# Kernel tuning notes

Hardware: AMD Instinct MI355X
Metric: run time of the kernel (lower is better)

Reference implementation:

```python
import jax, jax.numpy as jnp
import numpy as np

B, F, V, DW, H, K, T = 32, 2048, 12000, 300, 512, 3, 32
START_ID, END_ID = 1, 2
NEG = -1e9


def lstm(x, h, c, Wx, Wh, b):
    # BasicLSTMCell with forget_bias=1.0
    z = x @ Wx + h @ Wh + b  # [N, 4H]
    i, f, g, o = jnp.split(z, 4, axis=-1)
    c2 = jax.nn.sigmoid(f + 1.0) * c + jax.nn.sigmoid(i) * jnp.tanh(g)
    h2 = jax.nn.sigmoid(o) * jnp.tanh(c2)
    return h2, c2


def beam_decode(E, Wx, Wh, b, Wl, bl, img):
    Bn = img.shape[0]
    img_t = jnp.repeat(img, K, axis=0)  # tile_batch: [B*K, F]
    h = jnp.zeros((Bn * K, H), img.dtype)
    c = jnp.zeros_like(h)
    beam_lp = jnp.tile(jnp.array([0.0] + [NEG] * (K - 1), img.dtype), (Bn, 1))  # [B,K]
    prev = jnp.full((Bn, K), START_ID, jnp.int32)
    finished = jnp.zeros((Bn, K), bool)
    lengths = jnp.zeros((Bn, K), jnp.int32)
    ids = jnp.zeros((Bn, K, T), jnp.int32)
    end_row = jnp.where(jnp.arange(V) == END_ID, 0.0, NEG)  # finished beams only emit END

    def step(carry, t):
        h, c, beam_lp, prev, finished, lengths, ids = carry
        x = jnp.concatenate([E[prev.reshape(-1)], img_t], axis=-1)  # [B*K, DW+F]
        h2, c2 = lstm(x, h, c, Wx, Wh, b)
        lp = jax.nn.log_softmax(h2 @ Wl + bl).reshape(Bn, K, V)
        lp = jnp.where(finished[:, :, None], end_row, lp)
        total = (beam_lp[:, :, None] + lp).reshape(Bn, K * V)
        scores, idx = jax.lax.top_k(total, K)  # [B,K]
        parent = idx // V
        word = (idx % V).astype(jnp.int32)
        g2 = lambda a: jnp.take_along_axis(a, parent, axis=1)
        g3 = lambda a: jnp.take_along_axis(a, parent[:, :, None], axis=1)
        h2 = g3(h2.reshape(Bn, K, H)).reshape(Bn * K, H)
        c2 = g3(c2.reshape(Bn, K, H)).reshape(Bn * K, H)
        ids = g3(ids).at[:, :, t].set(word)  # reorder hypotheses, append word
        fin_p = g2(finished)
        len_p = g2(lengths)
        lengths = jnp.where(fin_p, len_p, len_p + 1)
        finished = fin_p | (word == END_ID)
        return (h2, c2, scores, word, finished, lengths, ids), None

    carry, _ = jax.lax.scan(step, (h, c, beam_lp, prev, finished, lengths, ids), jnp.arange(T))
    return carry[6], carry[5]  # ids [B,K,T], lengths [B,K]


def teacher_rnn(E, Wx, Wh, b, img_t, seq_inputs, lengths):
    # dynamic_rnn semantics: zero outputs and frozen state past sequence_length
    N, L = seq_inputs.shape
    emb = E[seq_inputs]  # [N, L, DW]
    h0 = jnp.zeros((N, H), E.dtype)
    c0 = jnp.zeros_like(h0)

    def step(carry, xs):
        h, c = carry
        x_t, t = xs
        xin = jnp.concatenate([x_t, img_t], axis=-1)
        h2, c2 = lstm(xin, h, c, Wx, Wh, b)
        active = (t < lengths)[:, None]
        h = jnp.where(active, h2, h)
        c = jnp.where(active, c2, c)
        return (h, c), jnp.where(active, h2, 0.0)

    _, outs = jax.lax.scan(step, (h0, c0), (emb.transpose(1, 0, 2), jnp.arange(L)))
    return outs.transpose(1, 0, 2)  # [N, L, H]


def setup_inputs() -> dict:
    key = jax.random.key(0)
    ks = jax.random.split(key, 6)
    return {
        "mean_image_features": jax.random.normal(ks[0], (B, F), jnp.float32),
        "embeddings": jax.random.normal(ks[1], (V, DW), jnp.float32) * 0.1,
        "Wx": jax.random.normal(ks[2], (DW + F, 4 * H), jnp.float32) / np.sqrt(DW + F),
        "Wh": jax.random.normal(ks[3], (H, 4 * H), jnp.float32) / np.sqrt(H),
        "b_lstm": jnp.zeros((4 * H,), jnp.float32),
        "W_logits": jax.random.normal(ks[4], (H, V), jnp.float32) / np.sqrt(H),
        "b_logits": jnp.zeros((V,), jnp.float32),
    }


def reference(mean_image_features, embeddings, Wx, Wh, b_lstm, W_logits, b_logits):
    Bn = mean_image_features.shape[0]
    ids, lengths = beam_decode(embeddings, Wx, Wh, b_lstm, W_logits, b_logits, mean_image_features)
    seq_inputs = jnp.concatenate(
        [jnp.full((Bn, K, 1), START_ID, jnp.int32), ids], axis=2
    ).reshape(Bn * K, T + 1)
    img_t = jnp.repeat(mean_image_features, K, axis=0)
    acts = teacher_rnn(embeddings, Wx, Wh, b_lstm, img_t, seq_inputs, lengths.reshape(-1))
    logits = (acts @ W_logits + b_logits).reshape(Bn, K, T + 1, V)
    return logits, jnp.argmax(logits, axis=-1).astype(jnp.int32)
```

## Files before the change

### kernel.cpp

```cpp
#include <hip/hip_runtime.h>
#include <hip/hip_bf16.h>
#include <math.h>

#define NB   32
#define FDIM 2048
#define VV   12000
#define DWW  300
#define HH   512
#define KW   3
#define TDEC 32
#define SEQ  33
#define NK   96
#define G4   2048
#define START_ID 1
#define END_ID   2
#define NROWS 3168
#define NLB   188
#define INTMX 0x7fffffff
#define FLOORF (-3.0e38f)
#define BAR_STRIDE 512
#define SHARD 64

typedef float f4v __attribute__((ext_vector_type(4)));
__device__ __forceinline__ void nt_store4(float* p, float4 v){
  f4v t; t.x=v.x; t.y=v.y; t.z=v.z; t.w=v.w;
  __builtin_nontemporal_store(t, (f4v*)p);
}

__device__ __forceinline__ float sigf(float x){ return 1.0f/(1.0f+expf(-x)); }

__device__ __forceinline__ unsigned short f2b(float x){
  __hip_bfloat16 b = __float2bfloat16(x);
  return *reinterpret_cast<unsigned short*>(&b);
}

__device__ __forceinline__ void ins3(float v, int i, float tv[3], int ti[3]){
  if (v > tv[0] || (v == tv[0] && i < ti[0])){
    tv[2]=tv[1]; ti[2]=ti[1]; tv[1]=tv[0]; ti[1]=ti[0]; tv[0]=v; ti[0]=i;
  } else if (v > tv[1] || (v == tv[1] && i < ti[1])){
    tv[2]=tv[1]; ti[2]=ti[1]; tv[1]=v; ti[1]=i;
  } else if (v > tv[2] || (v == tv[2] && i < ti[2])){
    tv[2]=v; ti[2]=i;
  }
}

__device__ __forceinline__ void flag_arrive(int* f, int bid){
  __hip_atomic_fetch_add(f + (bid&7)*SHARD, 1, __ATOMIC_RELEASE, __HIP_MEMORY_SCOPE_AGENT);
}
__device__ __forceinline__ void flag_wait(int* f, int target){
  if (threadIdx.x < 64){
    int lane = threadIdx.x;
    for (;;){
      int x = (lane<8) ? __hip_atomic_load(f + lane*SHARD, __ATOMIC_ACQUIRE, __HIP_MEMORY_SCOPE_AGENT) : 0;
      x += __shfl_xor(x,1); x += __shfl_xor(x,2); x += __shfl_xor(x,4);
      if (__shfl(x,0) >= target) break;
      __builtin_amdgcn_s_sleep(4);
    }
  }
  __syncthreads();
}

struct SArgs {
  const float *E, *Wx, *Wh, *Wl, *blog;
  float *P, *c2, *h2s, *zp, *partA, *beam_lp, *rowamax;
  int *prev, *finished, *lengths, *parst;
  int *cnt0, *cnt1;
  void *Lst;
};

__global__ __launch_bounds__(128) void k_pimg(const float* __restrict__ img,
                                              const float* __restrict__ Wx,
                                              float* __restrict__ parts)
{
  int colb = blockIdx.x, fb = blockIdx.y, tid = threadIdx.x;
  int col = colb*128 + tid;
  int f0 = fb*128;
  __shared__ float s_img[32][128];
  for (int r=0;r<32;r++) s_img[r][tid] = img[r*FDIM + f0 + tid];
  __syncthreads();
  float acc[32];
  #pragma unroll
  for (int r=0;r<32;r++) acc[r]=0.f;
  for (int f2=0; f2<128; ++f2){
    float w = Wx[(size_t)(DWW + f0 + f2)*G4 + col];
    #pragma unroll
    for (int r=0;r<32;r++) acc[r] += w * s_img[r][f2];
  }
  #pragma unroll
  for (int r=0;r<32;r++) parts[(size_t)fb*(32*G4) + r*G4 + col] = acc[r];
}

__global__ __launch_bounds__(512) void k_prep(const float* __restrict__ parts,
    const float* __restrict__ bls, const float* __restrict__ blog,
    float* __restrict__ P, float* __restrict__ beam_lp, int* __restrict__ prev,
    int* __restrict__ finished, int* __restrict__ lengths, int* __restrict__ cnts,
    float* __restrict__ bamax)
{
  int bid = blockIdx.x, tid = threadIdx.x;
  int gid = bid*512 + tid;
  float s = bls[gid & (G4-1)];
  for (int fb=0; fb<16; ++fb) s += parts[(size_t)fb*(32*G4) + gid];
  P[gid] = s;
  if (gid < 2*TDEC*BAR_STRIDE) cnts[gid] = 0;
  if (bid==0 && tid<NK){
    beam_lp[tid] = (tid%KW==0)?0.f:-1e9f;
    prev[tid]=START_ID; finished[tid]=0; lengths[tid]=0;
  }
  if (bid==2){
    __shared__ float s_rf[8]; __shared__ int s_ri[8];
    float bv=FLOORF; int bi=INTMX;
    for (int i=tid;i<VV;i+=512){
      float v=blog[i];
      if (v>bv || (v==bv && i<bi)){ bv=v; bi=i; }
    }
    #pragma unroll
    for (int d=1;d<64;d<<=1){
      float ov=__shfl_xor(bv,d); int oi=__shfl_xor(bi,d);
      if (ov>bv || (ov==bv && oi<bi)){ bv=ov; bi=oi; }
    }
    if ((tid&63)==0){ s_rf[tid>>6]=bv; s_ri[tid>>6]=bi; }
    __syncthreads();
    if (tid==0){
      for (int w=1;w<8;w++)
        if (s_rf[w]>bv || (s_rf[w]==bv && s_ri[w]<bi)){ bv=s_rf[w]; bi=s_ri[w]; }
      bamax[0] = (float)bi;
    }
  }
}

__global__ __launch_bounds__(512) void k_step1(SArgs a, int t)
{
  int bid = blockIdx.x, tid = threadIdx.x;
  __shared__ float smem[96*17 + 16*64];
  __shared__ int sprev[NK], spar[NK];
  if (t>0 && tid<NK){ sprev[tid]=a.prev[tid]; spar[tid]=a.parst[(t-1)*NK+tid]; }
  __syncthreads();

  {
    int colblk = bid & 31, p = bid >> 5;
    int col0 = colblk*64;
    int ks = p*104, ke = ks+104; if (ke>812) ke=812;
    float* sA = smem;
    float* sB = smem + 96*17;
    int tx = tid&15, ty = tid>>4;
    float4 acc[3];
    #pragma unroll
    for (int r=0;r<3;r++) acc[r]=make_float4(0.f,0.f,0.f,0.f);
    for (int k0=ks;k0<ke;k0+=16){
      int bk = ke-k0; if (bk>16) bk=16;
      for (int i=tid;i<96*16;i+=512){
        int n=i>>4, kk=i&15;
        float v=0.f;
        if (kk<bk){
          int kg=k0+kk;
          if (kg<DWW){
            int w = (t==0)?START_ID:sprev[n];
            v = a.E[(size_t)w*DWW+kg];
          } else if (t>0){
            v = a.h2s[((size_t)(t-1)*NK + spar[n])*HH + (kg-DWW)];
          }
        }
        sA[n*17+kk]=v;
      }
      for (int i=tid;i<16*64;i+=512){
        int kk=i>>6, cc=i&63;
        float v=0.f;
        if (kk<bk){
          int kg=k0+kk;
          v = (kg<DWW) ? a.Wx[(size_t)kg*G4+col0+cc] : a.Wh[(size_t)(kg-DWW)*G4+col0+cc];
        }
        sB[i]=v;
      }
      __syncthreads();
      #pragma unroll
      for (int kk=0;kk<16;++kk){
        float4 b4 = *(const float4*)&sB[kk*64+tx*4];
        #pragma unroll
        for (int rr=0;rr<3;rr++){
          float av = sA[(ty+rr*32)*17+kk];
          acc[rr].x += av*b4.x; acc[rr].y += av*b4.y;
          acc[rr].z += av*b4.z; acc[rr].w += av*b4.w;
        }
      }
      __syncthreads();
    }
    float* zpp = a.zp + (size_t)p*NK*G4;
    #pragma unroll
    for (int rr=0;rr<3;rr++)
      *(float4*)&zpp[(size_t)(ty+rr*32)*G4 + col0 + tx*4] = acc[rr];
  }
  __syncthreads();
  if (tid==0) flag_arrive(&a.cnt0[t*BAR_STRIDE], bid);
  if (bid >= NK) return;

  flag_wait(&a.cnt0[t*BAR_STRIDE], 256);
  {
    int n = bid, m = tid, bb = n/KW;
    const float* Pr = a.P + (size_t)bb*G4;
    float zi=Pr[m], zf=Pr[HH+m], zg=Pr[2*HH+m], zo=Pr[3*HH+m];
    for (int p=0;p<8;p++){
      const float* zz = a.zp + (size_t)p*NK*G4 + (size_t)n*G4;
      zi+=zz[m]; zf+=zz[HH+m]; zg+=zz[2*HH+m]; zo+=zz[3*HH+m];
    }
    float cold = (t==0) ? 0.f : a.c2[(size_t)((t-1)&1)*NK*HH + (size_t)spar[n]*HH + m];
    float c2v = sigf(zf+1.0f)*cold + sigf(zi)*tanhf(zg);
    float h2v = sigf(zo)*tanhf(c2v);
    a.c2[(size_t)(t&1)*NK*HH + (size_t)n*HH + m] = c2v;
    a.h2s[((size_t)t*NK+n)*HH + m] = h2v;
  }
}

template<int BF>
__global__ __launch_bounds__(512) void k_step2(SArgs a, int t)
{
  int bid = blockIdx.x, tid = threadIdx.x;
  __shared__ float smem[96*36 + 32*64];
  __shared__ float s_lse[KW], s_tv3[KW*3];
  __shared__ int   s_ti3[KW*3];

  {
    int col0 = bid*64;
    float* sA = smem;
    float* sB = smem + 96*36;
    int tx=tid&15, ty=tid>>4;
    float4 acc[3];
    #pragma unroll
    for (int r=0;r<3;r++) acc[r]=make_float4(0.f,0.f,0.f,0.f);
    for (int k0=0;k0<HH;k0+=32){
      for (int i=tid;i<768;i+=512){
        int row=i>>3, kq=(i&7)*4;
        *(float4*)&sA[row*36+kq] = *(const float4*)&a.h2s[((size_t)t*NK+row)*HH + k0+kq];
      }
      {
        int kk=tid>>4, c4=(tid&15)*4;
        int col=col0+c4;
        float4 v = make_float4(0.f,0.f,0.f,0.f);
        if (col < VV) v = *(const float4*)&a.Wl[(size_t)(k0+kk)*VV+col];
        *(float4*)&sB[kk*64+c4]=v;
      }
      __syncthreads();
      #pragma unroll
      for (int kk=0;kk<32;++kk){
        float4 b4 = *(const float4*)&sB[kk*64+tx*4];
        #pragma unroll
        for (int rr=0;rr<3;rr++){
          float av = sA[(ty+rr*32)*36+kk];
          acc[rr].x += av*b4.x; acc[rr].y += av*b4.y;
          acc[rr].z += av*b4.z; acc[rr].w += av*b4.w;
        }
      }
      __syncthreads();
    }
    int colg = col0 + tx*4;
    bool cval = colg < VV;
    float4 bias = make_float4(0.f,0.f,0.f,0.f);
    if (cval) bias = *(const float4*)&a.blog[colg];
    #pragma unroll
    for (int rr=0;rr<3;rr++){
      int row = ty + rr*32;
      float v0,v1,v2,v3;
      if (cval){
        v0=acc[rr].x+bias.x; v1=acc[rr].y+bias.y;
        v2=acc[rr].z+bias.z; v3=acc[rr].w+bias.w;
        size_t off = (size_t)(t*NK+row)*VV + colg;
        if (BF){
          ushort4 u;
          u.x=f2b(v0); u.y=f2b(v1); u.z=f2b(v2); u.w=f2b(v3);
          *(ushort4*)((unsigned short*)a.Lst + off) = u;
        } else {
          *(float4*)((float*)a.Lst + off) = make_float4(v0,v1,v2,v3);
        }
      } else { v0=v1=v2=v3=-INFINITY; }
      float m = fmaxf(fmaxf(v0,v1),fmaxf(v2,v3));
      #pragma unroll
      for (int d=1;d<16;d<<=1) m = fmaxf(m,__shfl_xor(m,d));
      float tv[3]={-INFINITY,-INFINITY,-INFINITY};
      int   ti[3]={INTMX,INTMX,INTMX};
      float s=0.f;
      if (cval){
        ins3(v0,colg,tv,ti); ins3(v1,colg+1,tv,ti);
        ins3(v2,colg+2,tv,ti); ins3(v3,colg+3,tv,ti);
        s = expf(v0-m)+expf(v1-m)+expf(v2-m)+expf(v3-m);
      }
      #pragma unroll
      for (int d=1;d<16;d<<=1){
        s += __shfl_xor(s,d);
        float p0=__shfl_xor(tv[0],d),p1=__shfl_xor(tv[1],d),p2=__shfl_xor(tv[2],d);
        int q0=__shfl_xor(ti[0],d),q1=__shfl_xor(ti[1],d),q2=__shfl_xor(ti[2],d);
        ins3(p0,q0,tv,ti); ins3(p1,q1,tv,ti); ins3(p2,q2,tv,ti);
      }
      if (tx==0){
        float* rp = a.partA + ((size_t)row*NLB + bid)*8;
        *(float4*)rp = make_float4(m,s,tv[0],tv[1]);
        *((float4*)rp+1) = make_float4(tv[2],__int_as_float(ti[0]),__int_as_float(ti[1]),__int_as_float(ti[2]));
      }
    }
  }
  __syncthreads();
  if (tid==0) flag_arrive(&a.cnt1[t*BAR_STRIDE], bid);
  if (bid >= NB) return;

  flag_wait(&a.cnt1[t*BAR_STRIDE], NLB);
  {
    int b = bid;
    int wv = tid>>6, lane = tid&63;
    if (wv < KW){
      int n = b*KW+wv;
      float M=FLOORF, S=0.f;
      float tv[3]={FLOORF,FLOORF,FLOORF}; int ti[3]={INTMX,INTMX,INTMX};
      for (int i=lane;i<NLB;i+=64){
        const float* rp = a.partA + ((size_t)n*NLB+i)*8;
        float4 r0=*(const float4*)rp, r1=*((const float4*)rp+1);
        float nm = fmaxf(M,r0.x);
        S = S*expf(M-nm) + r0.y*expf(r0.x-nm);
        M = nm;
        ins3(r0.z,__float_as_int(r1.y),tv,ti);
        ins3(r0.w,__float_as_int(r1.z),tv,ti);
        ins3(r1.x,__float_as_int(r1.w),tv,ti);
      }
      #pragma unroll
      for (int d=1;d<64;d<<=1){
        float Mo=__shfl_xor(M,d), So=__shfl_xor(S,d);
        float nm=fmaxf(M,Mo);
        S = S*expf(M-nm)+So*expf(Mo-nm);
        M=nm;
        float p0=__shfl_xor(tv[0],d),p1=__shfl_xor(tv[1],d),p2=__shfl_xor(tv[2],d);
        int q0=__shfl_xor(ti[0],d),q1=__shfl_xor(ti[1],d),q2=__shfl_xor(ti[2],d);
        ins3(p0,q0,tv,ti); ins3(p1,q1,tv,ti); ins3(p2,q2,tv,ti);
      }
      if (lane==0){
        s_lse[wv] = M + logf(S);
        #pragma unroll
        for (int j=0;j<3;j++){ s_tv3[wv*3+j]=tv[j]; s_ti3[wv*3+j]=ti[j]; }
        a.rowamax[t*NK+n] = (float)ti[0];
      }
    }
    __syncthreads();
    if (tid==0){
      float cv[3]={FLOORF,FLOORF,FLOORF}; int cf[3]={INTMX,INTMX,INTMX};
      for (int k=0;k<KW;k++){
        int n=b*KW+k;
        if (a.finished[n]){
          ins3(a.beam_lp[n], k*VV+END_ID, cv,cf);
        } else {
          float blp=a.beam_lp[n], lse=s_lse[k];
          for (int j=0;j<3;j++)
            ins3(blp + (s_tv3[k*3+j]-lse), k*VV+s_ti3[k*3+j], cv,cf);
        }
      }
      int fin_old[KW], len_old[KW];
      for (int j=0;j<KW;j++){ fin_old[j]=a.finished[b*KW+j]; len_old[j]=a.lengths[b*KW+j]; }
      for (int kp=0;kp<KW;kp++){
        int par=cf[kp]/VV, word=cf[kp]-par*VV;
        a.beam_lp[b*KW+kp]=cv[kp];
        a.prev[b*KW+kp]=word;
        a.parst[t*NK + b*KW+kp] = b*KW+par;
        int fp=fin_old[par];
        a.lengths[b*KW+kp] = fp?len_old[par]:(len_old[par]+1);
        a.finished[b*KW+kp] = fp | (word==END_ID);
      }
    }
  }
}

__global__ __launch_bounds__(128) void k_backtrack(const int* __restrict__ parst,
                                                   const int* __restrict__ lengths,
                                                   int* __restrict__ rowsrc)
{
  int n = threadIdx.x;
  if (n >= NK) return;
  int b = n / KW;
  int len = lengths[n];
  rowsrc[n*SEQ + TDEC] = -1;
  int a = n;
  for (int tau = TDEC-1; tau >= 1; --tau){
    int p = parst[tau*NK + a];
    rowsrc[n*SEQ + tau] = (tau < len) ? (tau*NK + p) : -1;
    a = p;
  }
  rowsrc[n*SEQ + 0] = b*KW;
}

template<int BF>
__global__ __launch_bounds__(512) void k_gather(const void* __restrict__ Lst,
    const int* __restrict__ rowsrc, const float* __restrict__ rowamax,
    const float* __restrict__ bamax, const float* __restrict__ blog,
    float* __restrict__ out)
{
  int row = blockIdx.x, tid = threadIdx.x;
  int src = rowsrc[row];
  float* orow = out + (size_t)row*VV;
  if (src >= 0){
    if (BF){
      const unsigned short* L = (const unsigned short*)Lst + (size_t)src*VV;
      for (int j=tid;j<VV/4;j+=512){
        ushort4 u = *(const ushort4*)&L[j*4];
        float4 v;
        v.x = __uint_as_float(((unsigned)u.x)<<16);
        v.y = __uint_as_float(((unsigned)u.y)<<16);
        v.z = __uint_as_float(((unsigned)u.z)<<16);
        v.w = __uint_as_float(((unsigned)u.w)<<16);
        nt_store4(&orow[j*4], v);
      }
    } else {
      const float* L = (const float*)Lst + (size_t)src*VV;
      for (int j=tid;j<VV/4;j+=512){
        float4 v = *(const float4*)&L[j*4];
        nt_store4(&orow[j*4], v);
      }
    }
    if (tid==0) out[(size_t)NROWS*VV + row] = rowamax[src];
  } else {
    for (int j=tid;j<VV/4;j+=512){
      float4 v = *(const float4*)&blog[j*4];
      nt_store4(&orow[j*4], v);
    }
    if (tid==0) out[(size_t)NROWS*VV + row] = bamax[0];
  }
}

extern "C" void kernel_launch(void* const* d_in, const int* in_sizes, int n_in,
                              void* d_out, int out_size, void* d_ws, size_t ws_size,
                              hipStream_t stream) {
  (void)in_sizes; (void)n_in; (void)out_size;
  const float* img  = (const float*)d_in[0];
  const float* E    = (const float*)d_in[1];
  const float* Wx   = (const float*)d_in[2];
  const float* Wh   = (const float*)d_in[3];
  const float* bls  = (const float*)d_in[4];
  const float* Wl   = (const float*)d_in[5];
  const float* blog = (const float*)d_in[6];
  float* out = (float*)d_out;

  float* ws = (float*)d_ws;
  size_t o = 0;
  float* P       = ws+o; o += (size_t)NB*G4;
  float* c2      = ws+o; o += (size_t)2*NK*HH;
  float* h2s     = ws+o; o += (size_t)TDEC*NK*HH;
  float* zp      = ws+o; o += (size_t)8*NK*G4;
  float* partA   = ws+o; o += (size_t)NK*NLB*8;
  float* beam_lp = ws+o; o += 128;
  float* rowamax = ws+o; o += (size_t)TDEC*NK;
  float* bamax   = ws+o; o += 4;
  int* prev      = (int*)(ws+o); o += 128;
  int* finished  = (int*)(ws+o); o += 128;
  int* lengths   = (int*)(ws+o); o += 128;
  int* parst     = (int*)(ws+o); o += (size_t)TDEC*NK;
  int* rowsrc    = (int*)(ws+o); o += 3328;
  int* cnts      = (int*)(ws+o); o += (size_t)2*TDEC*BAR_STRIDE;
  o = (o+3) & ~(size_t)3;
  void* Lst      = (void*)(ws+o);

  bool f32 = (ws_size/4 > o) && ((ws_size/4 - o) >= (size_t)TDEC*NK*VV);

  SArgs a;
  a.E=E; a.Wx=Wx; a.Wh=Wh; a.Wl=Wl; a.blog=blog;
  a.P=P; a.c2=c2; a.h2s=h2s; a.zp=zp; a.partA=partA;
  a.beam_lp=beam_lp; a.rowamax=rowamax;
  a.prev=prev; a.finished=finished; a.lengths=lengths; a.parst=parst;
  a.cnt0=cnts; a.cnt1=cnts+TDEC*BAR_STRIDE;
  a.Lst=Lst;

  k_pimg<<<dim3(16,16),128,0,stream>>>(img, Wx, zp);
  k_prep<<<128,512,0,stream>>>(zp, bls, blog, P, beam_lp, prev, finished, lengths, cnts, bamax);

  if (f32){
    for (int t=0;t<TDEC;t++){
      k_step1<<<256,512,0,stream>>>(a,t);
      k_step2<0><<<NLB,512,0,stream>>>(a,t);
    }
    k_backtrack<<<1,128,0,stream>>>(parst, lengths, rowsrc);
    k_gather<0><<<NROWS,512,0,stream>>>(Lst,rowsrc,rowamax,bamax,blog,out);
  } else {
    for (int t=0;t<TDEC;t++){
      k_step1<<<256,512,0,stream>>>(a,t);
      k_step2<1><<<NLB,512,0,stream>>>(a,t);
    }
    k_backtrack<<<1,128,0,stream>>>(parst, lengths, rowsrc);
    k_gather<1><<<NROWS,512,0,stream>>>(Lst,rowsrc,rowamax,bamax,blog,out);
  }
}
```

Measured before the change: 2.961 ms.

## Fuse per-step LSTM and logits kernels into one launch with flag barriers

Merges k_step1 and k_step2 into a single k_step kernel per decode step. The two stages are now joined by an in-kernel atomic flag barrier instead of a kernel boundary, and the backtrack is folded into the last step behind another barrier. This drops 33 kernel launches and their inter-kernel gaps. The flag-wait loop now polls with relaxed loads and a shorter sleep, then does one acquire load at the end. The cost is a larger shared-memory footprint for the fused kernel and reliance on all 188 participating blocks being co-resident to avoid deadlock.

Measured after the change: 3.093 ms. 4.5% more time.

```diff
diff --git a/kernel.cpp b/kernel.cpp
--- a/kernel.cpp
+++ b/kernel.cpp
@@ -20,6 +20,7 @@
 #define FLOORF (-3.0e38f)
 #define BAR_STRIDE 512
 #define SHARD 64
+#define NBAR (3*TDEC+1)
 
 typedef float f4v __attribute__((ext_vector_type(4)));
 __device__ __forceinline__ void nt_store4(float* p, float4 v){
@@ -51,11 +52,12 @@
   if (threadIdx.x < 64){
     int lane = threadIdx.x;
     for (;;){
-      int x = (lane<8) ? __hip_atomic_load(f + lane*SHARD, __ATOMIC_ACQUIRE, __HIP_MEMORY_SCOPE_AGENT) : 0;
+      int x = (lane<8) ? __hip_atomic_load(f + lane*SHARD, __ATOMIC_RELAXED, __HIP_MEMORY_SCOPE_AGENT) : 0;
       x += __shfl_xor(x,1); x += __shfl_xor(x,2); x += __shfl_xor(x,4);
       if (__shfl(x,0) >= target) break;
-      __builtin_amdgcn_s_sleep(4);
-    }
+      __builtin_amdgcn_s_sleep(2);
+    }
+    if (lane==0) (void)__hip_atomic_load(f, __ATOMIC_ACQUIRE, __HIP_MEMORY_SCOPE_AGENT);
   }
   __syncthreads();
 }
@@ -63,8 +65,8 @@
 struct SArgs {
   const float *E, *Wx, *Wh, *Wl, *blog;
   float *P, *c2, *h2s, *zp, *partA, *beam_lp, *rowamax;
-  int *prev, *finished, *lengths, *parst;
-  int *cnt0, *cnt1;
+  int *prev, *finished, *lengths, *parst, *rowsrc;
+  int *cnts;
   void *Lst;
 };
 
@@ -101,7 +103,7 @@
   float s = bls[gid & (G4-1)];
   for (int fb=0; fb<16; ++fb) s += parts[(size_t)fb*(32*G4) + gid];
   P[gid] = s;
-  if (gid < 2*TDEC*BAR_STRIDE) cnts[gid] = 0;
+  if (gid < NBAR*BAR_STRIDE) cnts[gid] = 0;
   if (bid==0 && tid<NK){
     beam_lp[tid] = (tid%KW==0)?0.f:-1e9f;
     prev[tid]=START_ID; finished[tid]=0; lengths[tid]=0;
@@ -128,11 +130,19 @@
   }
 }
 
-__global__ __launch_bounds__(512) void k_step1(SArgs a, int t)
+template<int BF>
+__global__ __launch_bounds__(512) void k_step(SArgs a, int t)
 {
   int bid = blockIdx.x, tid = threadIdx.x;
-  __shared__ float smem[96*17 + 16*64];
+  __shared__ float smem[96*36 + 32*64];
   __shared__ int sprev[NK], spar[NK];
+  __shared__ float s_lse[KW], s_tv3[KW*3];
+  __shared__ int   s_ti3[KW*3];
+  int* bZ = a.cnts + (size_t)(t*3+0)*BAR_STRIDE;
+  int* bG = a.cnts + (size_t)(t*3+1)*BAR_STRIDE;
+  int* bL = a.cnts + (size_t)(t*3+2)*BAR_STRIDE;
+  int* bS = a.cnts + (size_t)(3*TDEC)*BAR_STRIDE;
+
   if (t>0 && tid<NK){ sprev[tid]=a.prev[tid]; spar[tid]=a.parst[(t-1)*NK+tid]; }
   __syncthreads();
 
@@ -190,11 +200,11 @@
       *(float4*)&zpp[(size_t)(ty+rr*32)*G4 + col0 + tx*4] = acc[rr];
   }
   __syncthreads();
-  if (tid==0) flag_arrive(&a.cnt0[t*BAR_STRIDE], bid);
-  if (bid >= NK) return;
-
-  flag_wait(&a.cnt0[t*BAR_STRIDE], 256);
-  {
+  if (tid==0) flag_arrive(bZ, bid);
+  if (bid >= NLB) return;
+
+  if (bid < NK){
+    flag_wait(bZ, 256);
     int n = bid, m = tid, bb = n/KW;
     const float* Pr = a.P + (size_t)bb*G4;
     float zi=Pr[m], zf=Pr[HH+m], zg=Pr[2*HH+m], zo=Pr[3*HH+m];
@@ -207,18 +217,12 @@
     float h2v = sigf(zo)*tanhf(c2v);
     a.c2[(size_t)(t&1)*NK*HH + (size_t)n*HH + m] = c2v;
     a.h2s[((size_t)t*NK+n)*HH + m] = h2v;
-  }
-}
-
-template<int BF>
-__global__ __launch_bounds__(512) void k_step2(SArgs a, int t)
-{
-  int bid = blockIdx.x, tid = threadIdx.x;
-  __shared__ float smem[96*36 + 32*64];
-  __shared__ float s_lse[KW], s_tv3[KW*3];
-  __shared__ int   s_ti3[KW*3];
+    __syncthreads();
+    if (tid==0) flag_arrive(bG, bid);
+  }
 
   {
+    flag_wait(bG, NK);
     int col0 = bid*64;
     float* sA = smem;
     float* sB = smem + 96*36;
@@ -297,10 +301,10 @@
     }
   }
   __syncthreads();
-  if (tid==0) flag_arrive(&a.cnt1[t*BAR_STRIDE], bid);
+  if (tid==0) flag_arrive(bL, bid);
   if (bid >= NB) return;
 
-  flag_wait(&a.cnt1[t*BAR_STRIDE], NLB);
+  flag_wait(bL, NLB);
   {
     int b = bid;
     int wv = tid>>6, lane = tid&63;
@@ -361,24 +365,26 @@
       }
     }
   }
-}
-
-__global__ __launch_bounds__(128) void k_backtrack(const int* __restrict__ parst,
-                                                   const int* __restrict__ lengths,
-                                                   int* __restrict__ rowsrc)
-{
-  int n = threadIdx.x;
-  if (n >= NK) return;
-  int b = n / KW;
-  int len = lengths[n];
-  rowsrc[n*SEQ + TDEC] = -1;
-  int a = n;
-  for (int tau = TDEC-1; tau >= 1; --tau){
-    int p = parst[tau*NK + a];
-    rowsrc[n*SEQ + tau] = (tau < len) ? (tau*NK + p) : -1;
-    a = p;
-  }
-  rowsrc[n*SEQ + 0] = b*KW;
+
+  if (t == TDEC-1){
+    __syncthreads();
+    if (tid==0) flag_arrive(bS, bid);
+    if (bid==0){
+      flag_wait(bS, NB);
+      if (tid<NK){
+        int n=tid, b=n/KW;
+        int len = a.lengths[n];
+        a.rowsrc[n*SEQ+TDEC] = -1;
+        int cur=n;
+        for (int tau=TDEC-1; tau>=1; --tau){
+          int p = a.parst[tau*NK+cur];
+          a.rowsrc[n*SEQ+tau] = (tau<len) ? (tau*NK+p) : -1;
+          cur=p;
+        }
+        a.rowsrc[n*SEQ+0] = b*KW;
+      }
+    }
+  }
 }
 
 template<int BF>
@@ -447,7 +453,7 @@
   int* lengths   = (int*)(ws+o); o += 128;
   int* parst     = (int*)(ws+o); o += (size_t)TDEC*NK;
   int* rowsrc    = (int*)(ws+o); o += 3328;
-  int* cnts      = (int*)(ws+o); o += (size_t)2*TDEC*BAR_STRIDE;
+  int* cnts      = (int*)(ws+o); o += (size_t)NBAR*BAR_STRIDE;
   o = (o+3) & ~(size_t)3;
   void* Lst      = (void*)(ws+o);
 
@@ -457,26 +463,18 @@
   a.E=E; a.Wx=Wx; a.Wh=Wh; a.Wl=Wl; a.blog=blog;
   a.P=P; a.c2=c2; a.h2s=h2s; a.zp=zp; a.partA=partA;
   a.beam_lp=beam_lp; a.rowamax=rowamax;
-  a.prev=prev; a.finished=finished; a.lengths=lengths; a.parst=parst;
-  a.cnt0=cnts; a.cnt1=cnts+TDEC*BAR_STRIDE;
+  a.prev=prev; a.finished=finished; a.lengths=lengths; a.parst=parst; a.rowsrc=rowsrc;
+  a.cnts=cnts;
   a.Lst=Lst;
 
   k_pimg<<<dim3(16,16),128,0,stream>>>(img, Wx, zp);
   k_prep<<<128,512,0,stream>>>(zp, bls, blog, P, beam_lp, prev, finished, lengths, cnts, bamax);
 
   if (f32){
-    for (int t=0;t<TDEC;t++){
-      k_step1<<<256,512,0,stream>>>(a,t);
-      k_step2<0><<<NLB,512,0,stream>>>(a,t);
-    }
-    k_backtrack<<<1,128,0,stream>>>(parst, lengths, rowsrc);
+    for (int t=0;t<TDEC;t++) k_step<0><<<256,512,0,stream>>>(a,t);
     k_gather<0><<<NROWS,512,0,stream>>>(Lst,rowsrc,rowamax,bamax,blog,out);
   } else {
-    for (int t=0;t<TDEC;t++){
-      k_step1<<<256,512,0,stream>>>(a,t);
-      k_step2<1><<<NLB,512,0,stream>>>(a,t);
-    }
-    k_backtrack<<<1,128,0,stream>>>(parst, lengths, rowsrc);
+    for (int t=0;t<TDEC;t++) k_step<1><<<256,512,0,stream>>>(a,t);
     k_gather<1><<<NROWS,512,0,stream>>>(Lst,rowsrc,rowamax,bamax,blog,out);
   }
 }
```
